# Kernel optimization log

Measured on AMD Instinct MI355X. Metric: run time of the kernel, lower is better.

Reference implementation:

```python
import jax, jax.numpy as jnp
import numpy as np
from jax.scipy.special import logsumexp

D = 256; H = 8; A = D // H
B_CONST = 0.9; P_MAX = 50000.0; P_MIN = 1e-4; TANH_RATE = 0.005; EPS = 1e-10
SCALE = 1.0 / np.sqrt(D)


def setup_inputs() -> dict:
    key = jax.random.key(0)
    ks = jax.random.split(key, 5)
    B, S = 2, 512
    context = jax.random.normal(ks[0], (B, S, D), dtype=jnp.float32)
    W_Q = jax.random.normal(ks[1], (D, D), dtype=jnp.float32) * (1.0 / np.sqrt(D))
    W_KV = jax.random.normal(ks[2], (2 * D, D), dtype=jnp.float32) * (1.0 / np.sqrt(D))
    W_out = jax.random.normal(ks[3], (D, D), dtype=jnp.float32) * (1.0 / np.sqrt(D))
    p_param = jax.random.normal(ks[4], (D,), dtype=jnp.float32) * 0.02
    return {"context": context, "W_Q": W_Q, "W_KV": W_KV, "W_out": W_out, "p_param": p_param}


def reference(context, W_Q, W_KV, W_out, p_param):
    B, S, _ = context.shape
    # projections (nn.Linear: x @ W.T)
    q = context @ W_Q.T                          # [B,S,D]
    kv = context @ W_KV.T                        # [B,S,2D]
    k, v = kv[..., :D], kv[..., D:]
    # scaled p: p_max*tanh(tanh_rate*p)+1, then replace exact zeros with p_min
    p = P_MAX * jnp.tanh(TANH_RATE * p_param) + 1.0
    p = p + (p == 0).astype(p.dtype) * P_MIN
    # minmax-normalize v over the key/sequence axis into [b, 1]
    v_max = jnp.max(v, axis=-2, keepdims=True)   # [B,1,D]
    v_min = jnp.min(v, axis=-2, keepdims=True)
    v = (1.0 - B_CONST) * (v - v_min) / (v_max - v_min + EPS) + B_CONST
    z = p * jnp.log(v)                           # [B,S,D]
    # split heads
    qh = q.reshape(B, S, H, A).transpose(0, 2, 1, 3)          # [B,H,S,A]
    kh = k.reshape(B, S, H, A).transpose(0, 2, 1, 3)          # [B,H,S,A]
    zh = z.reshape(B, S, H, A).transpose(0, 2, 1, 3)[:, :, None]  # [B,H,1,K,A]
    dot = jnp.einsum('bhqa,bhka->bhqk', qh, kh)
    w = jax.nn.log_softmax(dot * SCALE, axis=-1)              # [B,H,Q,K]
    # log-domain power mean: logsumexp over keys of log-weights + p*log(v)
    mean = logsumexp(w[..., None] + zh, axis=-2)              # [B,H,Q,A]
    mean = mean.transpose(0, 2, 1, 3).reshape(B, S, D)
    e = jnp.exp(mean / p)
    # invert v minmax normalization
    e = (e - B_CONST) * (v_max - v_min + EPS) / (1.0 - B_CONST) + v_min
    return e @ W_out.T
```

## Files before the change

### kernel.cpp

```cpp
#include <hip/hip_runtime.h>
#include <math.h>

#define DD 256
#define HH 8
#define AA 32
#define SS 512
#define BB 2
constexpr float BCONST      = 0.9f;
constexpr float ONE_MINUS_B = 0.1f;
constexpr float EPSF        = 1e-10f;
constexpr float SCALEF      = 0.0625f;
constexpr float FLTMAX      = 3.402823466e38f;

#define OFF_QKV    0
#define OFF_VP     786432
#define OFF_EW     1048576
#define OFF_PMIN   1310720
#define OFF_PMAX   1318912
#define OFF_VMIN   1327104
#define OFF_VRANGE 1327616
#define OFF_P      1328128

#define KB4(buf, row, col4) \
  (&(buf)[((row) << 5) | ((((col4) >> 2) ^ (((row) >> 2) & 7)) << 2)])

template<int TM, int TN, int RM, int RN, bool MM>
__global__ __launch_bounds__(256) void gemm_t(
    const float* __restrict__ A, const float* __restrict__ B0,
    const float* __restrict__ B1, int nsplit,
    float* __restrict__ C, int ldc, int K, int lda,
    float* __restrict__ pminP, float* __restrict__ pmaxP) {
  constexpr int LDT = 36;
  constexpr int CG  = TN / RN;
  constexpr int NA  = TM * 32 / 1024;
  constexpr int NB  = TN * 32 / 1024;
  __shared__ float As[TM][LDT];
  __shared__ float Bs[TN][LDT];
  const int i0 = blockIdx.x * TM;
  const int j0 = blockIdx.y * TN;
  const float* Bsrc = (j0 < nsplit) ? (B0 + (size_t)j0 * K)
                                    : (B1 + (size_t)(j0 - nsplit) * K);
  const int t  = threadIdx.x;
  const int lr = t >> 3;
  const int lc = (t & 7) << 2;
  const int tx = t % CG, ty = t / CG;

  float4 pa[NA], pb[NB];
#pragma unroll
  for (int u = 0; u < NA; ++u)
    pa[u] = *(const float4*)(A + (size_t)(i0 + lr + 32 * u) * lda + lc);
#pragma unroll
  for (int u = 0; u < NB; ++u)
    pb[u] = *(const float4*)(Bsrc + (size_t)(lr + 32 * u) * K + lc);

  float acc[RM][RN] = {};
  for (int k0 = 0; k0 < K; k0 += 32) {
    __syncthreads();
#pragma unroll
    for (int u = 0; u < NA; ++u) *(float4*)&As[lr + 32 * u][lc] = pa[u];
#pragma unroll
    for (int u = 0; u < NB; ++u) *(float4*)&Bs[lr + 32 * u][lc] = pb[u];
    __syncthreads();
    if (k0 + 32 < K) {
#pragma unroll
      for (int u = 0; u < NA; ++u)
        pa[u] = *(const float4*)(A + (size_t)(i0 + lr + 32 * u) * lda + k0 + 32 + lc);
#pragma unroll
      for (int u = 0; u < NB; ++u)
        pb[u] = *(const float4*)(Bsrc + (size_t)(lr + 32 * u) * K + k0 + 32 + lc);
    }
#pragma unroll
    for (int kk = 0; kk < 32; kk += 4) {
      float4 af[RM], bf[RN];
#pragma unroll
      for (int r = 0; r < RM; ++r) af[r] = *(const float4*)&As[ty * RM + r][kk];
#pragma unroll
      for (int c = 0; c < RN; ++c) bf[c] = *(const float4*)&Bs[tx + CG * c][kk];
#pragma unroll
      for (int r = 0; r < RM; ++r)
#pragma unroll
        for (int c = 0; c < RN; ++c)
          acc[r][c] += af[r].x * bf[c].x + af[r].y * bf[c].y +
                       af[r].z * bf[c].z + af[r].w * bf[c].w;
    }
  }
#pragma unroll
  for (int r = 0; r < RM; ++r)
#pragma unroll
    for (int c = 0; c < RN; ++c)
      C[(size_t)(i0 + ty * RM + r) * ldc + j0 + tx + CG * c] = acc[r][c];

  if (MM && j0 >= 512) {
    __syncthreads();
    float* mnb = &As[0][0];
    float* mxb = &Bs[0][0];
#pragma unroll
    for (int c = 0; c < RN; ++c) {
      float mn = acc[0][c], mx = acc[0][c];
#pragma unroll
      for (int r = 1; r < RM; ++r) {
        mn = fminf(mn, acc[r][c]);
        mx = fmaxf(mx, acc[r][c]);
      }
      mnb[(tx + CG * c) * 17 + ty] = mn;
      mxb[(tx + CG * c) * 17 + ty] = mx;
    }
    __syncthreads();
    if (t < TN) {
      float mn = mnb[t * 17], mx = mxb[t * 17];
#pragma unroll
      for (int i = 1; i < 16; ++i) {
        mn = fminf(mn, mnb[t * 17 + i]);
        mx = fmaxf(mx, mxb[t * 17 + i]);
      }
      const int bx = i0 >> 5;
      pminP[bx * 256 + (j0 - 512) + t] = mn;
      pmaxP[bx * 256 + (j0 - 512) + t] = mx;
    }
  }
}

__global__ __launch_bounds__(256) void vpk(
    const float* __restrict__ qkv, const float* __restrict__ pminP,
    const float* __restrict__ pmaxP, const float* __restrict__ p_param,
    float* __restrict__ vp, float* __restrict__ vminw,
    float* __restrict__ vrangew, float* __restrict__ pw) {
  const int blk = blockIdx.x;
  const int b = blk >> 9, s = blk & 511;
  const int d = threadIdx.x;
  float mn = pminP[(b * 16) * 256 + d];
  float mx = pmaxP[(b * 16) * 256 + d];
#pragma unroll
  for (int c = 1; c < 16; ++c) {
    mn = fminf(mn, pminP[(b * 16 + c) * 256 + d]);
    mx = fmaxf(mx, pmaxP[(b * 16 + c) * 256 + d]);
  }
  float p = 50000.0f * tanhf(0.005f * p_param[d]) + 1.0f;
  if (p == 0.0f) p = 0.0001f;
  const float range = mx - mn + EPSF;
  const float v  = qkv[((size_t)(b * 512 + s)) * 768 + 512 + d];
  const float vn = (ONE_MINUS_B * (v - mn)) / range + BCONST;
  vp[(size_t)blk * 256 + d] = expm1f(p * logf(vn));
  if (s == 0) { vminw[b * 256 + d] = mn; vrangew[b * 256 + d] = range; }
  if (blk == 0) pw[d] = p;
}

__global__ __launch_bounds__(256) void attn_k(
    const float* __restrict__ qkv, const float* __restrict__ vp,
    const float* __restrict__ pw, const float* __restrict__ vminw,
    const float* __restrict__ vrangew, float* __restrict__ ew) {
  __shared__ float qs[16][36];
  __shared__ float scT[512 * 20];
  __shared__ float kb[256 * 32];
  __shared__ float red[16][17];
  const int bh  = blockIdx.x;
  const int b   = bh >> 3, h = bh & 7;
  const int q0g = blockIdx.y * 16;
  const int t   = threadIdx.x;
  const int ldr = t >> 3, ldc4 = (t & 7) << 2;

  if (t < 128) {
    const int q = t >> 3, c4 = (t & 7) << 2;
    float4 qv = *(const float4*)(qkv + ((size_t)(b * 512 + q0g + q)) * 768 + h * 32 + c4);
    qv.x *= SCALEF; qv.y *= SCALEF; qv.z *= SCALEF; qv.w *= SCALEF;
    *(float4*)&qs[q][c4] = qv;
  }

  float4 pk[8];
#pragma unroll 2
  for (int u = 0; u < 8; ++u)
    pk[u] = *(const float4*)(qkv + ((size_t)(b * 512 + ldr + 32 * u)) * 768 + 256 + h * 32 + ldc4);

  const int qg = t & 3;
  const int kg = t >> 2;
  for (int kc = 0; kc < 2; ++kc) {
    __syncthreads();
#pragma unroll 2
    for (int u = 0; u < 8; ++u) *(float4*)KB4(kb, ldr + 32 * u, ldc4) = pk[u];
    __syncthreads();
    if (kc == 0) {
#pragma unroll 2
      for (int u = 0; u < 8; ++u)
        pk[u] = *(const float4*)(qkv + ((size_t)(b * 512 + 256 + ldr + 32 * u)) * 768 + 256 + h * 32 + ldc4);
    } else {
#pragma unroll 2
      for (int u = 0; u < 8; ++u)
        pk[u] = *(const float4*)(vp + ((size_t)(b * 512 + ldr + 32 * u)) * 256 + h * 32 + ldc4);
    }
    float a2[4][4] = {};
#pragma unroll 2
    for (int kk = 0; kk < 32; kk += 4) {
      float4 qf[4], kf[4];
#pragma unroll
      for (int r = 0; r < 4; ++r) qf[r] = *(const float4*)&qs[qg * 4 + r][kk];
#pragma unroll
      for (int c = 0; c < 4; ++c) kf[c] = *(const float4*)KB4(kb, kg * 4 + c, kk);
#pragma unroll
      for (int r = 0; r < 4; ++r)
#pragma unroll
        for (int c = 0; c < 4; ++c)
          a2[r][c] += qf[r].x * kf[c].x + qf[r].y * kf[c].y +
                      qf[r].z * kf[c].z + qf[r].w * kf[c].w;
    }
#pragma unroll
    for (int c = 0; c < 4; ++c)
      *(float4*)&scT[(kc * 256 + kg * 4 + c) * 20 + qg * 4] =
          make_float4(a2[0][c], a2[1][c], a2[2][c], a2[3][c]);
  }
  __syncthreads();

  {
    const int q = t & 15, j = t >> 4;
    float m = -FLTMAX;
#pragma unroll 4
    for (int i = 0; i < 32; ++i) m = fmaxf(m, scT[(j * 32 + i) * 20 + q]);
    red[q][j] = m;
    __syncthreads();
    float rm = red[q][0];
#pragma unroll 4
    for (int jj = 1; jj < 16; ++jj) rm = fmaxf(rm, red[q][jj]);
    __syncthreads();
    float ls = 0.f;
#pragma unroll 4
    for (int i = 0; i < 32; ++i) {
      float e = __expf(scT[(j * 32 + i) * 20 + q] - rm);
      scT[(j * 32 + i) * 20 + q] = e;
      ls += e;
    }
    red[q][j] = ls;
    __syncthreads();
    if (j == 0) {
      float tot = 0.f;
#pragma unroll 4
      for (int jj = 0; jj < 16; ++jj) tot += red[q][jj];
      red[q][16] = tot;
    }
  }

  float a3[4][4] = {};
  const int qg3 = t & 3;
  const int ag3 = (t >> 2) & 7;
  const int ks  = t >> 5;
  for (int kc = 0; kc < 2; ++kc) {
    __syncthreads();
#pragma unroll 2
    for (int u = 0; u < 8; ++u) *(float4*)KB4(kb, ldr + 32 * u, ldc4) = pk[u];
    __syncthreads();
    if (kc == 0) {
#pragma unroll 2
      for (int u = 0; u < 8; ++u)
        pk[u] = *(const float4*)(vp + ((size_t)(b * 512 + 256 + ldr + 32 * u)) * 256 + h * 32 + ldc4);
    }
#pragma unroll 2
    for (int g = 0; g < 8; ++g) {
#pragma unroll
      for (int c = 0; c < 4; ++c) {
        const int k = ks * 32 + g * 4 + c;
        const float4 sq = *(const float4*)&scT[(kc * 256 + k) * 20 + qg3 * 4];
        const float4 vf = *(const float4*)KB4(kb, k, ag3 * 4);
        a3[0][0] += sq.x * vf.x; a3[0][1] += sq.x * vf.y; a3[0][2] += sq.x * vf.z; a3[0][3] += sq.x * vf.w;
        a3[1][0] += sq.y * vf.x; a3[1][1] += sq.y * vf.y; a3[1][2] += sq.y * vf.z; a3[1][3] += sq.y * vf.w;
        a3[2][0] += sq.z * vf.x; a3[2][1] += sq.z * vf.y; a3[2][2] += sq.z * vf.z; a3[2][3] += sq.z * vf.w;
        a3[3][0] += sq.w * vf.x; a3[3][1] += sq.w * vf.y; a3[3][2] += sq.w * vf.z; a3[3][3] += sq.w * vf.w;
      }
    }
  }

#pragma unroll
  for (int r = 0; r < 4; ++r)
#pragma unroll
    for (int c = 0; c < 4; ++c)
      a3[r][c] += __shfl_xor(a3[r][c], 32);
  __syncthreads();
  float* part2 = &kb[0];
  if ((t & 32) == 0) {
    const int w = t >> 6;
#pragma unroll
    for (int r = 0; r < 4; ++r)
#pragma unroll
      for (int c = 0; c < 4; ++c)
        part2[w * 520 + (qg3 * 4 + r) * 32 + ag3 * 4 + c] = a3[r][c];
  }
  __syncthreads();
  {
    const int q = t >> 4, a = (t * 2) & 31;
    const float invT = 1.0f / red[q][16];
    float o2[2];
#pragma unroll
    for (int o = 0; o < 2; ++o) {
      const int ia = q * 32 + a + o;
      float s = part2[ia] + part2[520 + ia] + part2[1040 + ia] + part2[1560 + ia];
      s *= invT;
      const int d = h * 32 + a + o;
      const float p = pw[d];
      const float mean = log1pf(s);
      const float en = expf(mean / p);
      o2[o] = (en - BCONST) * vrangew[b * 256 + d] / ONE_MINUS_B + vminw[b * 256 + d];
    }
    *(float2*)(ew + ((size_t)(b * 512 + q0g + q)) * 256 + h * 32 + a) =
        make_float2(o2[0], o2[1]);
  }
}

extern "C" void kernel_launch(void* const* d_in, const int* in_sizes, int n_in,
                              void* d_out, int out_size, void* d_ws, size_t ws_size,
                              hipStream_t stream) {
  const float* ctx  = (const float*)d_in[0];
  const float* WQ   = (const float*)d_in[1];
  const float* WKV  = (const float*)d_in[2];
  const float* WOUT = (const float*)d_in[3];
  const float* PP   = (const float*)d_in[4];
  float* ws      = (float*)d_ws;
  float* qkv     = ws + OFF_QKV;
  float* vp      = ws + OFF_VP;
  float* ew      = ws + OFF_EW;
  float* pminP   = ws + OFF_PMIN;
  float* pmaxP   = ws + OFF_PMAX;
  float* vminw   = ws + OFF_VMIN;
  float* vrangew = ws + OFF_VRANGE;
  float* pw      = ws + OFF_P;
  float* out     = (float*)d_out;

  gemm_t<32, 64, 2, 4, true><<<dim3(32, 12), 256, 0, stream>>>(
      ctx, WQ, WKV, 256, qkv, 768, 256, 256, pminP, pmaxP);
  vpk<<<1024, 256, 0, stream>>>(qkv, pminP, pmaxP, PP, vp, vminw, vrangew, pw);
  attn_k<<<dim3(16, 32), 256, 0, stream>>>(qkv, vp, pw, vminw, vrangew, ew);
  gemm_t<32, 32, 2, 2, false><<<dim3(32, 8), 256, 0, stream>>>(
      ew, WOUT, WOUT, 1 << 30, out, 256, 256, 256, nullptr, nullptr);
}
```

Before: 120.2 us.

## Double attention query tile to 32 and stage all 512 keys in LDS at once

The attention kernel now handles 32 queries per block instead of 16 and loads all 512 K rows (then V rows) into shared memory in one pass, dropping the two-chunk register-prefetch pipeline. Scores are stored row-major per query, and softmax and the PV product use wider float4 reads with 8x4 register tiles per thread. The epilogue is vectorised to float4 stores. This halves the grid and the redundant K/V reloads per head, at the cost of much larger LDS use (about 134 KB), which limits occupancy and removes the load/compute overlap.

```diff
diff --git a/kernel.cpp b/kernel.cpp
--- a/kernel.cpp
+++ b/kernel.cpp
@@ -149,156 +149,163 @@
     const float* __restrict__ qkv, const float* __restrict__ vp,
     const float* __restrict__ pw, const float* __restrict__ vminw,
     const float* __restrict__ vrangew, float* __restrict__ ew) {
-  __shared__ float qs[16][36];
-  __shared__ float scT[512 * 20];
-  __shared__ float kb[256 * 32];
-  __shared__ float red[16][17];
-  const int bh  = blockIdx.x;
+  __shared__ float qs[32][36];
+  __shared__ float sc[32 * 516];
+  __shared__ float kb[512 * 32];
+  __shared__ float red[32][9];
+  const int bh  = blockIdx.y;
   const int b   = bh >> 3, h = bh & 7;
-  const int q0g = blockIdx.y * 16;
+  const int q0g = blockIdx.x * 32;
   const int t   = threadIdx.x;
-  const int ldr = t >> 3, ldc4 = (t & 7) << 2;
-
-  if (t < 128) {
+  const int srow = t >> 3, scol4 = (t & 7) << 2;
+
+  {
     const int q = t >> 3, c4 = (t & 7) << 2;
     float4 qv = *(const float4*)(qkv + ((size_t)(b * 512 + q0g + q)) * 768 + h * 32 + c4);
     qv.x *= SCALEF; qv.y *= SCALEF; qv.z *= SCALEF; qv.w *= SCALEF;
     *(float4*)&qs[q][c4] = qv;
   }
-
-  float4 pk[8];
-#pragma unroll 2
-  for (int u = 0; u < 8; ++u)
-    pk[u] = *(const float4*)(qkv + ((size_t)(b * 512 + ldr + 32 * u)) * 768 + 256 + h * 32 + ldc4);
-
-  const int qg = t & 3;
-  const int kg = t >> 2;
-  for (int kc = 0; kc < 2; ++kc) {
-    __syncthreads();
-#pragma unroll 2
-    for (int u = 0; u < 8; ++u) *(float4*)KB4(kb, ldr + 32 * u, ldc4) = pk[u];
-    __syncthreads();
-    if (kc == 0) {
-#pragma unroll 2
-      for (int u = 0; u < 8; ++u)
-        pk[u] = *(const float4*)(qkv + ((size_t)(b * 512 + 256 + ldr + 32 * u)) * 768 + 256 + h * 32 + ldc4);
-    } else {
-#pragma unroll 2
-      for (int u = 0; u < 8; ++u)
-        pk[u] = *(const float4*)(vp + ((size_t)(b * 512 + ldr + 32 * u)) * 256 + h * 32 + ldc4);
-    }
-    float a2[4][4] = {};
+#pragma unroll 8
+  for (int u = 0; u < 16; ++u) {
+    const int r = srow + 32 * u;
+    float4 v = *(const float4*)(qkv + ((size_t)(b * 512 + r)) * 768 + 256 + h * 32 + scol4);
+    *(float4*)KB4(kb, r, scol4) = v;
+  }
+  __syncthreads();
+
+  {
+    const int qgw = t >> 6;
+    const int kg  = t & 63;
+    float s8[8][8] = {};
 #pragma unroll 2
     for (int kk = 0; kk < 32; kk += 4) {
-      float4 qf[4], kf[4];
-#pragma unroll
-      for (int r = 0; r < 4; ++r) qf[r] = *(const float4*)&qs[qg * 4 + r][kk];
-#pragma unroll
-      for (int c = 0; c < 4; ++c) kf[c] = *(const float4*)KB4(kb, kg * 4 + c, kk);
-#pragma unroll
-      for (int r = 0; r < 4; ++r)
-#pragma unroll
-        for (int c = 0; c < 4; ++c)
-          a2[r][c] += qf[r].x * kf[c].x + qf[r].y * kf[c].y +
-                      qf[r].z * kf[c].z + qf[r].w * kf[c].w;
-    }
-#pragma unroll
-    for (int c = 0; c < 4; ++c)
-      *(float4*)&scT[(kc * 256 + kg * 4 + c) * 20 + qg * 4] =
-          make_float4(a2[0][c], a2[1][c], a2[2][c], a2[3][c]);
+      float4 qf[8], kf1[4], kf2[4];
+#pragma unroll
+      for (int r = 0; r < 8; ++r) qf[r] = *(const float4*)&qs[qgw + 4 * r][kk];
+#pragma unroll
+      for (int c = 0; c < 4; ++c) {
+        kf1[c] = *(const float4*)KB4(kb, kg * 4 + c, kk);
+        kf2[c] = *(const float4*)KB4(kb, 256 + kg * 4 + c, kk);
+      }
+#pragma unroll
+      for (int r = 0; r < 8; ++r)
+#pragma unroll
+        for (int c = 0; c < 4; ++c) {
+          s8[r][c]     += qf[r].x * kf1[c].x + qf[r].y * kf1[c].y +
+                          qf[r].z * kf1[c].z + qf[r].w * kf1[c].w;
+          s8[r][4 + c] += qf[r].x * kf2[c].x + qf[r].y * kf2[c].y +
+                          qf[r].z * kf2[c].z + qf[r].w * kf2[c].w;
+        }
+    }
+#pragma unroll
+    for (int r = 0; r < 8; ++r) {
+      const int rq = qgw + 4 * r;
+      *(float4*)&sc[rq * 516 + kg * 4] =
+          make_float4(s8[r][0], s8[r][1], s8[r][2], s8[r][3]);
+      *(float4*)&sc[rq * 516 + 256 + kg * 4] =
+          make_float4(s8[r][4], s8[r][5], s8[r][6], s8[r][7]);
+    }
   }
   __syncthreads();
 
   {
-    const int q = t & 15, j = t >> 4;
+    const int q = t & 31, j = t >> 5;
     float m = -FLTMAX;
 #pragma unroll 4
-    for (int i = 0; i < 32; ++i) m = fmaxf(m, scT[(j * 32 + i) * 20 + q]);
+    for (int g = 0; g < 16; ++g) {
+      float4 x = *(const float4*)&sc[q * 516 + j * 64 + 4 * g];
+      m = fmaxf(m, fmaxf(fmaxf(x.x, x.y), fmaxf(x.z, x.w)));
+    }
     red[q][j] = m;
     __syncthreads();
     float rm = red[q][0];
-#pragma unroll 4
-    for (int jj = 1; jj < 16; ++jj) rm = fmaxf(rm, red[q][jj]);
+#pragma unroll
+    for (int jj = 1; jj < 8; ++jj) rm = fmaxf(rm, red[q][jj]);
     __syncthreads();
     float ls = 0.f;
 #pragma unroll 4
-    for (int i = 0; i < 32; ++i) {
-      float e = __expf(scT[(j * 32 + i) * 20 + q] - rm);
-      scT[(j * 32 + i) * 20 + q] = e;
-      ls += e;
+    for (int g = 0; g < 16; ++g) {
+      float4 x = *(const float4*)&sc[q * 516 + j * 64 + 4 * g];
+      x.x = __expf(x.x - rm); x.y = __expf(x.y - rm);
+      x.z = __expf(x.z - rm); x.w = __expf(x.w - rm);
+      *(float4*)&sc[q * 516 + j * 64 + 4 * g] = x;
+      ls += x.x + x.y + x.z + x.w;
     }
     red[q][j] = ls;
     __syncthreads();
     if (j == 0) {
       float tot = 0.f;
-#pragma unroll 4
-      for (int jj = 0; jj < 16; ++jj) tot += red[q][jj];
-      red[q][16] = tot;
-    }
-  }
-
-  float a3[4][4] = {};
-  const int qg3 = t & 3;
-  const int ag3 = (t >> 2) & 7;
+#pragma unroll
+      for (int jj = 0; jj < 8; ++jj) tot += red[q][jj];
+      red[q][8] = tot;
+    }
+  }
+
+#pragma unroll 8
+  for (int u = 0; u < 16; ++u) {
+    const int r = srow + 32 * u;
+    float4 v = *(const float4*)(vp + ((size_t)(b * 512 + r)) * 256 + h * 32 + scol4);
+    *(float4*)KB4(kb, r, scol4) = v;
+  }
+  __syncthreads();
+
+  const int ag  = t & 7;
+  const int qg3 = (t >> 3) & 3;
   const int ks  = t >> 5;
-  for (int kc = 0; kc < 2; ++kc) {
-    __syncthreads();
+  float a3[8][4] = {};
 #pragma unroll 2
-    for (int u = 0; u < 8; ++u) *(float4*)KB4(kb, ldr + 32 * u, ldc4) = pk[u];
-    __syncthreads();
-    if (kc == 0) {
-#pragma unroll 2
-      for (int u = 0; u < 8; ++u)
-        pk[u] = *(const float4*)(vp + ((size_t)(b * 512 + 256 + ldr + 32 * u)) * 256 + h * 32 + ldc4);
-    }
-#pragma unroll 2
-    for (int g = 0; g < 8; ++g) {
-#pragma unroll
-      for (int c = 0; c < 4; ++c) {
-        const int k = ks * 32 + g * 4 + c;
-        const float4 sq = *(const float4*)&scT[(kc * 256 + k) * 20 + qg3 * 4];
-        const float4 vf = *(const float4*)KB4(kb, k, ag3 * 4);
-        a3[0][0] += sq.x * vf.x; a3[0][1] += sq.x * vf.y; a3[0][2] += sq.x * vf.z; a3[0][3] += sq.x * vf.w;
-        a3[1][0] += sq.y * vf.x; a3[1][1] += sq.y * vf.y; a3[1][2] += sq.y * vf.z; a3[1][3] += sq.y * vf.w;
-        a3[2][0] += sq.z * vf.x; a3[2][1] += sq.z * vf.y; a3[2][2] += sq.z * vf.z; a3[2][3] += sq.z * vf.w;
-        a3[3][0] += sq.w * vf.x; a3[3][1] += sq.w * vf.y; a3[3][2] += sq.w * vf.z; a3[3][3] += sq.w * vf.w;
-      }
-    }
-  }
-
-#pragma unroll
-  for (int r = 0; r < 4; ++r)
+  for (int g = 0; g < 16; ++g) {
+    const int kbase = ks * 64 + g * 4;
+    float4 sq[8], vf[4];
+#pragma unroll
+    for (int r = 0; r < 8; ++r)
+      sq[r] = *(const float4*)&sc[(qg3 + 4 * r) * 516 + kbase];
+#pragma unroll
+    for (int c = 0; c < 4; ++c)
+      vf[c] = *(const float4*)KB4(kb, kbase + c, ag * 4);
+#pragma unroll
+    for (int r = 0; r < 8; ++r) {
+      a3[r][0] += sq[r].x * vf[0].x + sq[r].y * vf[1].x + sq[r].z * vf[2].x + sq[r].w * vf[3].x;
+      a3[r][1] += sq[r].x * vf[0].y + sq[r].y * vf[1].y + sq[r].z * vf[2].y + sq[r].w * vf[3].y;
+      a3[r][2] += sq[r].x * vf[0].z + sq[r].y * vf[1].z + sq[r].z * vf[2].z + sq[r].w * vf[3].z;
+      a3[r][3] += sq[r].x * vf[0].w + sq[r].y * vf[1].w + sq[r].z * vf[2].w + sq[r].w * vf[3].w;
+    }
+  }
+
+#pragma unroll
+  for (int r = 0; r < 8; ++r)
 #pragma unroll
     for (int c = 0; c < 4; ++c)
       a3[r][c] += __shfl_xor(a3[r][c], 32);
   __syncthreads();
-  float* part2 = &kb[0];
+  float* part = &kb[0];
   if ((t & 32) == 0) {
     const int w = t >> 6;
 #pragma unroll
-    for (int r = 0; r < 4; ++r)
+    for (int r = 0; r < 8; ++r)
 #pragma unroll
       for (int c = 0; c < 4; ++c)
-        part2[w * 520 + (qg3 * 4 + r) * 32 + ag3 * 4 + c] = a3[r][c];
-  }
-  __syncthreads();
+        part[w * 1152 + (qg3 + 4 * r) * 36 + ag * 4 + c] = a3[r][c];
+  }
+  __syncthreads();
+
   {
-    const int q = t >> 4, a = (t * 2) & 31;
-    const float invT = 1.0f / red[q][16];
-    float o2[2];
-#pragma unroll
-    for (int o = 0; o < 2; ++o) {
-      const int ia = q * 32 + a + o;
-      float s = part2[ia] + part2[520 + ia] + part2[1040 + ia] + part2[1560 + ia];
-      s *= invT;
-      const int d = h * 32 + a + o;
-      const float p = pw[d];
-      const float mean = log1pf(s);
-      const float en = expf(mean / p);
-      o2[o] = (en - BCONST) * vrangew[b * 256 + d] / ONE_MINUS_B + vminw[b * 256 + d];
-    }
-    *(float2*)(ew + ((size_t)(b * 512 + q0g + q)) * 256 + h * 32 + a) =
-        make_float2(o2[0], o2[1]);
+    const int q = t >> 3, a0 = (t & 7) << 2;
+    const int d0 = h * 32 + a0;
+    const float invT = 1.0f / red[q][8];
+    float4 s0 = *(const float4*)&part[q * 36 + a0];
+    float4 s1 = *(const float4*)&part[1152 + q * 36 + a0];
+    float4 s2 = *(const float4*)&part[2304 + q * 36 + a0];
+    float4 s3 = *(const float4*)&part[3456 + q * 36 + a0];
+    const float4 pp = *(const float4*)(pw + d0);
+    const float4 vr = *(const float4*)(vrangew + b * 256 + d0);
+    const float4 vm = *(const float4*)(vminw + b * 256 + d0);
+    float4 o;
+    o.x = (expf(log1pf((s0.x + s1.x + s2.x + s3.x) * invT) / pp.x) - BCONST) * vr.x / ONE_MINUS_B + vm.x;
+    o.y = (expf(log1pf((s0.y + s1.y + s2.y + s3.y) * invT) / pp.y) - BCONST) * vr.y / ONE_MINUS_B + vm.y;
+    o.z = (expf(log1pf((s0.z + s1.z + s2.z + s3.z) * invT) / pp.z) - BCONST) * vr.z / ONE_MINUS_B + vm.z;
+    o.w = (expf(log1pf((s0.w + s1.w + s2.w + s3.w) * invT) / pp.w) - BCONST) * vr.w / ONE_MINUS_B + vm.w;
+    *(float4*)(ew + ((size_t)(b * 512 + q0g + q)) * 256 + d0) = o;
   }
 }
 
@@ -324,7 +331,7 @@
   gemm_t<32, 64, 2, 4, true><<<dim3(32, 12), 256, 0, stream>>>(
       ctx, WQ, WKV, 256, qkv, 768, 256, 256, pminP, pmaxP);
   vpk<<<1024, 256, 0, stream>>>(qkv, pminP, pmaxP, PP, vp, vminw, vrangew, pw);
-  attn_k<<<dim3(16, 32), 256, 0, stream>>>(qkv, vp, pw, vminw, vrangew, ew);
+  attn_k<<<dim3(16, 16), 256, 0, stream>>>(qkv, vp, pw, vminw, vrangew, ew);
   gemm_t<32, 32, 2, 2, false><<<dim3(32, 8), 256, 0, stream>>>(
       ew, WOUT, WOUT, 1 << 30, out, 256, 256, 256, nullptr, nullptr);
 }
```

After: 109.8 us. 8.6% less time.
